# Performance work log

Measured on AMD Instinct MI355X. Metric: run time of the kernel, lower is better.

The kernel has to match this reference:

```python
import jax, jax.numpy as jnp
import numpy as np

H = 12          # nheads
SIM_EPS = 1e-8  # SimMatrix eps
LN_EPS = 1e-5   # nn.LayerNorm default eps
SLOPE = 0.01    # LeakyReLU default negative slope


def leaky(x):
    return jnp.where(x >= 0, x, SLOPE * x)


def etc_attention(hiddens, gamma, beta, Wout, bout):
    # hiddens: [B, L, 3*D]
    B, L, D3 = hiddens.shape
    D = D3 // 3
    d = D // H
    h = hiddens.reshape(B, L, 3, H, d)
    Q = h[:, :, 0].transpose(0, 2, 1, 3)  # [B,H,L,d]
    K = h[:, :, 1].transpose(0, 2, 1, 3)
    V = h[:, :, 2].transpose(0, 2, 1, 3)
    # cosine-similarity attention scores (SimMatrix(K, Q))
    Kn = K / jnp.clip(jnp.linalg.norm(K, axis=-1, keepdims=True), SIM_EPS, None)
    Qn = Q / jnp.clip(jnp.linalg.norm(Q, axis=-1, keepdims=True), SIM_EPS, None)
    att = jnp.einsum('bhid,bhjd->bhij', Kn, Qn)  # [B,H,L,L]
    # LayerNorm over the head axis H (lnormalize: [B, L*L, H] layernorm on last dim)
    mu = att.mean(axis=1, keepdims=True)
    var = att.var(axis=1, keepdims=True)  # biased, matches torch LayerNorm
    att = (att - mu) / jnp.sqrt(var + LN_EPS)
    att = att * gamma[None, :, None, None] + beta[None, :, None, None]
    att = jax.nn.softmax(att, axis=-1)
    att = jnp.where(jnp.isnan(att), jnp.zeros_like(att), att)  # removeNaN
    out = jnp.einsum('bhij,bhjd->bhid', att, V)          # att @ V
    out = out.transpose(0, 2, 1, 3).reshape(B, L, D)      # catHiddens
    # dropout is identity at inference; lin_out = Linear + Softmax
    probs = jax.nn.softmax(out @ Wout.T + bout, axis=-1)  # [B,L,C]
    return probs, att


def get_weights(att, masks):
    # att: [B,H,L,L], masks: [B,L] float
    w = masks * att.mean(axis=1).sum(axis=1)  # [B,L]
    return jax.nn.softmax(w, axis=-1)[..., None]  # [B,L,1]


def setup_inputs() -> dict:
    key = jax.random.key(0)
    ks = jax.random.split(key, 16)
    B, L = 16, 512
    Din, D, C, VOCAB = 300, 768, 20, 32000

    def kaiming(k, shape, fan_in):
        return jax.random.normal(k, shape, jnp.float32) * np.sqrt(2.0 / fan_in)

    return {
        'input_ids': jax.random.randint(ks[0], (B, L), 0, VOCAB),
        'wv': jax.random.normal(ks[1], (B, L, Din), jnp.float32),
        'emb': jax.random.normal(ks[2], (VOCAB, D), jnp.float32),
        'W_t': kaiming(ks[3], (3 * D, D), D),
        'b_t': jnp.zeros((3 * D,), jnp.float32),
        'gamma_t': jnp.ones((H,), jnp.float32),
        'beta_t': jnp.zeros((H,), jnp.float32),
        'Wout_t': kaiming(ks[4], (C, D), D),
        'bout_t': jnp.zeros((C,), jnp.float32),
        'W_h': kaiming(ks[5], (3 * D, Din), Din),
        'b_h': jnp.zeros((3 * D,), jnp.float32),
        'gamma_h': jnp.ones((H,), jnp.float32),
        'beta_h': jnp.zeros((H,), jnp.float32),
        'Wout_h': kaiming(ks[6], (C, D), D),
        'bout_h': jnp.zeros((C,), jnp.float32),
    }


def reference(input_ids, wv, emb, W_t, b_t, gamma_t, beta_t, Wout_t, bout_t,
              W_h, b_h, gamma_h, beta_h, Wout_h, bout_h):
    masks = (input_ids != 0).astype(jnp.float32)  # [B,L]
    # token branch: Embedding -> LeakyReLU -> Linear -> LeakyReLU
    h_t = leaky(leaky(emb[input_ids]) @ W_t.T + b_t)
    probs_t, att_t = etc_attention(h_t, gamma_t, beta_t, Wout_t, bout_t)
    probs_t = (get_weights(att_t, masks) * probs_t).sum(axis=1)  # [B,C]
    # hidden/word-vector branch: Linear -> LeakyReLU
    h_h = leaky(wv @ W_h.T + b_h)
    probs_h, att_h = etc_attention(h_h, gamma_h, beta_h, Wout_h, bout_h)
    probs_h = (get_weights(att_h, masks) * probs_h).sum(axis=1)
    return (probs_t + probs_h) / 2.0
```

## Files before the change

kernel.cpp:

```cpp
#include <hip/hip_runtime.h>

typedef unsigned int uint;
typedef unsigned short ushort;
typedef _Float16 f16;
typedef _Float16 h8 __attribute__((ext_vector_type(8)));
typedef float f32x4 __attribute__((ext_vector_type(4)));


__device__ __forceinline__ float b2f(ushort u){ return __uint_as_float(((uint)u)<<16); }
__device__ __forceinline__ ushort f2b(float f){
  uint u = __float_as_uint(f);
  uint r = u + 0x7fffu + ((u>>16)&1u);
  return (ushort)(r>>16);
}
__device__ __forceinline__ float leaky(float x){ return x >= 0.f ? x : 0.01f*x; }
__device__ __forceinline__ float ldf(const void* p, int idx, int isb){
  return isb ? b2f(((const ushort*)p)[idx]) : ((const float*)p)[idx];
}

#define GLOAD16(gp, lp) __builtin_amdgcn_global_load_lds( \
    (const __attribute__((address_space(1))) void*)(gp), \
    (__attribute__((address_space(3))) void*)(lp), 16, 0, 0)

__global__ __launch_bounds__(256) void k_init(const ushort* __restrict__ wvbits,
    int* __restrict__ flag, float* __restrict__ zbase){
  int bid = blockIdx.x, tid = threadIdx.x;
  if (bid == 0){
    if (tid == 0){
      int sane = 0;
      for (int i=0;i<128;i++){
        uint e = (wvbits[i]>>7)&0xffu;
        if (e==0u || (e>=90u && e<=150u)) sane++;
      }
      *flag = (sane >= 115) ? 1 : 0;
    }
  } else {
    zbase[(bid-1)*256 + tid] = 0.f;
  }
}

__global__ __launch_bounds__(256) void k_prep_all(const int* __restrict__ ids,
    const void* __restrict__ emb, const void* __restrict__ wv,
    const void* __restrict__ W0, const void* __restrict__ W1,
    const int* __restrict__ flag,
    f16* __restrict__ AhA, f16* __restrict__ WhA,
    f16* __restrict__ AhB, f16* __restrict__ WhB,
    int nBX, int nW0, int nA1, int nW1){
  int isb = *flag;
  int bx = blockIdx.x, tid = threadIdx.x;
  if (bx < nBX){
    int t = bx*256 + tid;
    int m = t / 96, kk = (t % 96) * 8;
    float o[8];
    if (isb){
      const ushort* src = (const ushort*)emb + (size_t)ids[m]*768 + kk;
      uint4 v = *(const uint4*)src;
      o[0]=__uint_as_float((v.x&0xffffu)<<16); o[1]=__uint_as_float(v.x&0xffff0000u);
      o[2]=__uint_as_float((v.y&0xffffu)<<16); o[3]=__uint_as_float(v.y&0xffff0000u);
      o[4]=__uint_as_float((v.z&0xffffu)<<16); o[5]=__uint_as_float(v.z&0xffff0000u);
      o[6]=__uint_as_float((v.w&0xffffu)<<16); o[7]=__uint_as_float(v.w&0xffff0000u);
    } else {
      const float* src = (const float*)emb + (size_t)ids[m]*768 + kk;
      float4 v0 = ((const float4*)src)[0];
      float4 v1 = ((const float4*)src)[1];
      o[0]=v0.x; o[1]=v0.y; o[2]=v0.z; o[3]=v0.w;
      o[4]=v1.x; o[5]=v1.y; o[6]=v1.z; o[7]=v1.w;
    }
    h8 hv;
    #pragma unroll
    for (int i=0;i<8;i++) hv[i] = (f16)leaky(o[i]);
    *(h8*)(AhA + (size_t)m*768 + kk) = hv;
  } else if (bx < nBX + nW0){
    int t = (bx - nBX)*256 + tid;
    int n = t / 96, kk = (t % 96) * 8;
    h8 hv;
    #pragma unroll
    for (int i=0;i<8;i++) hv[i] = (f16)ldf(W0, n*768 + kk + i, isb);
    *(h8*)(WhA + (size_t)n*768 + kk) = hv;
  } else if (bx < nBX + nW0 + nA1){
    int t = (bx - nBX - nW0)*256 + tid;
    int n = t / 40, kk = (t % 40) * 8;
    h8 hv;
    #pragma unroll
    for (int i=0;i<8;i++){
      int k = kk + i;
      hv[i] = (k < 300) ? (f16)ldf(wv, n*300 + k, isb) : (f16)0.f;
    }
    *(h8*)(AhB + (size_t)n*320 + kk) = hv;
  } else {
    int t = (bx - nBX - nW0 - nA1)*256 + tid;
    int n = t / 40, kk = (t % 40) * 8;
    h8 hv;
    #pragma unroll
    for (int i=0;i<8;i++){
      int k = kk + i;
      hv[i] = (k < 300) ? (f16)ldf(W1, n*300 + k, isb) : (f16)0.f;
    }
    *(h8*)(WhB + (size_t)n*320 + kk) = hv;
  }
}

__global__ __launch_bounds__(256) void k_gemm_m(
    const f16* AhA, const f16* WhA, const void* biasA, int KA,
    f16* QhA, f16* KhA, f16* VtA,
    const f16* AhB, const f16* WhB, const void* biasB, int KB,
    f16* QhB, f16* KhB, f16* VtB,
    const int* __restrict__ flag, int sbase){
  __shared__ __align__(16) f16 As[128*64];
  __shared__ __align__(16) f16 Bs[128*64];
  int z = sbase + blockIdx.z;
  const f16* Ah = z ? AhB : AhA;
  const f16* Wh = z ? WhB : WhA;
  const void* bias = z ? biasB : biasA;
  int KP = z ? KB : KA;
  f16* Qh = z ? QhB : QhA;
  f16* Kh = z ? KhB : KhA;
  f16* Vt = z ? VtB : VtA;
  int STEPS = KP >> 6;

  int tid = threadIdx.x;
  int w = tid >> 6, lane = tid & 63;
  int mrow = lane & 15, kq = lane >> 4;
  int m0 = blockIdx.x * 128;
  int n0 = blockIdx.y * 128;
  int msub = (w & 1) * 64, nsub = (w >> 1) * 64;

  f32x4 acc[4][4];
  #pragma unroll
  for (int mt=0; mt<4; mt++)
    #pragma unroll
    for (int nt=0; nt<4; nt++) acc[mt][nt] = (f32x4){0.f,0.f,0.f,0.f};

  int cbase = w*64 + lane;

  for (int step=0; step<STEPS; step++){
    int k0 = step*64;
    __syncthreads();
    #pragma unroll
    for (int rep=0; rep<4; rep++){
      int cb = rep*256 + w*64;
      int c  = rep*256 + cbase;
      int row = c >> 3;
      int qs  = (c & 7) ^ (row & 7);
      GLOAD16(Ah + (size_t)(m0+row)*KP + k0 + qs*8, As + cb*8);
      GLOAD16(Wh + (size_t)(n0+row)*KP + k0 + qs*8, Bs + cb*8);
    }
    __syncthreads();
    #pragma unroll
    for (int ks=0; ks<2; ks++){
      h8 af[4], bf[4];
      #pragma unroll
      for (int mt=0; mt<4; mt++){
        int row = msub + mt*16 + mrow;
        int slot = (ks*4 + kq) ^ (row & 7);
        af[mt] = *(const h8*)(As + row*64 + slot*8);
      }
      #pragma unroll
      for (int nt=0; nt<4; nt++){
        int row = nsub + nt*16 + mrow;
        int slot = (ks*4 + kq) ^ (row & 7);
        bf[nt] = *(const h8*)(Bs + row*64 + slot*8);
      }
      #pragma unroll
      for (int mt=0; mt<4; mt++)
        #pragma unroll
        for (int nt=0; nt<4; nt++)
          acc[mt][nt] = __builtin_amdgcn_mfma_f32_16x16x32_f16(af[mt], bf[nt], acc[mt][nt], 0, 0, 0);
    }
  }

  int isb = *flag;
  int n0w = n0 + nsub;
  int s = n0w / 768;
  int h = (n0w % 768) >> 6;
  float bv[4];
  #pragma unroll
  for (int nt=0; nt<4; nt++) bv[nt] = ldf(bias, n0w + nt*16 + mrow, isb);

  #pragma unroll
  for (int mt=0; mt<4; mt++){
    float yv[4][4];
    #pragma unroll
    for (int nt=0; nt<4; nt++)
      #pragma unroll
      for (int r=0; r<4; r++)
        yv[nt][r] = leaky(acc[mt][nt][r] + bv[nt]);
    if (s < 2){
      #pragma unroll
      for (int r=0; r<4; r++){
        float ss = yv[0][r]*yv[0][r] + yv[1][r]*yv[1][r]
                 + yv[2][r]*yv[2][r] + yv[3][r]*yv[3][r];
        ss += __shfl_xor(ss, 1); ss += __shfl_xor(ss, 2);
        ss += __shfl_xor(ss, 4); ss += __shfl_xor(ss, 8);
        float rn = 1.f / fmaxf(sqrtf(ss), 1e-8f);
        #pragma unroll
        for (int nt=0; nt<4; nt++) yv[nt][r] *= rn;
      }
    }
    #pragma unroll
    for (int nt=0; nt<4; nt++){
      #pragma unroll
      for (int r=0; r<4; r++){
        int m = m0 + msub + mt*16 + kq*4 + r;
        int dd = nt*16 + mrow;
        int bq = m >> 9, l = m & 511;
        float y = yv[nt][r];
        if (s == 0)      Qh[((size_t)(bq*12 + h)*512 + l)*64 + dd] = (f16)y;
        else if (s == 1) Kh[((size_t)(bq*12 + h)*512 + l)*64 + dd] = (f16)y;
        else             Vt[((size_t)(bq*12 + h)*64 + dd)*512 + l] = (f16)y;
      }
    }
  }
}

__global__ __launch_bounds__(256) void k_scores(const f16* __restrict__ Qh,
    const f16* __restrict__ Kh, const void* __restrict__ gamma,
    const void* __restrict__ beta, const int* __restrict__ flag,
    f16* __restrict__ E, float* __restrict__ lsump){
  constexpr int TS = 72;
  __shared__ f16 S[12*16*TS];
  __shared__ float gL[12], beL[12];

  int tid = threadIdx.x;
  int w = tid >> 6, lane = tid & 63;
  int kq = lane >> 4, mrow = lane & 15;
  int bx = (blockIdx.x & 7)*512 + (blockIdx.x >> 3);
  int jt = bx & 7, it = (bx >> 3) & 31, b = bx >> 8;
  int i0 = it*16, j0 = jt*64;

  if (tid < 12){ int isb = *flag; gL[tid] = ldf(gamma, tid, isb); beL[tid] = ldf(beta, tid, isb); }

  #pragma unroll
  for (int hh=0; hh<3; hh++){
    int h = w*3 + hh;
    const f16* kb = Kh + ((size_t)(b*12+h)*512 + i0 + mrow)*64;
    h8 a0 = *(const h8*)(kb + kq*8);
    h8 a1 = *(const h8*)(kb + 32 + kq*8);
    const f16* qb = Qh + ((size_t)(b*12+h)*512 + j0)*64;
    #pragma unroll
    for (int jn=0; jn<4; jn++){
      const f16* qr = qb + (size_t)(jn*16 + mrow)*64;
      h8 q0 = *(const h8*)(qr + kq*8);
      h8 q1 = *(const h8*)(qr + 32 + kq*8);
      f32x4 c = (f32x4){0.f,0.f,0.f,0.f};
      c = __builtin_amdgcn_mfma_f32_16x16x32_f16(a0, q0, c, 0, 0, 0);
      c = __builtin_amdgcn_mfma_f32_16x16x32_f16(a1, q1, c, 0, 0, 0);
      #pragma unroll
      for (int r=0;r<4;r++)
        S[(h*16 + kq*4 + r)*TS + jn*16 + mrow] = (f16)c[r];
    }
  }
  __syncthreads();
  int pj = tid & 63, piw = tid >> 6;
  #pragma unroll
  for (int p=0; p<4; p++){
    int i = piw*4 + p;
    float s[12];
    float mu = 0.f, sq = 0.f;
    #pragma unroll
    for (int h=0;h<12;h++){ s[h] = (float)S[(h*16+i)*TS + pj]; mu += s[h]; sq += s[h]*s[h]; }
    mu *= (1.f/12.f);
    float var = fmaxf(sq*(1.f/12.f) - mu*mu, 0.f);
    float rstd = rsqrtf(var + 1e-5f);
    #pragma unroll
    for (int h=0;h<12;h++){
      float e = __expf((s[h]-mu)*rstd*gL[h] + beL[h]);
      S[(h*16+i)*TS + pj] = (f16)e;
    }
  }
  __syncthreads();
  if (tid < 192){
    int h = tid >> 4, i = tid & 15;
    const f16* zr = &S[(h*16 + i)*TS];
    float ssum = 0.f;
    #pragma unroll
    for (int q=0;q<8;q++){
      h8 v = *(const h8*)(zr + q*8);
      #pragma unroll
      for (int t=0;t<8;t++) ssum += (float)v[t];
    }
    lsump[((size_t)(b*12+h)*512 + i0 + i)*8 + jt] = ssum;
  }
  #pragma unroll
  for (int u0=0; u0<6; u0++){
    int u = tid + u0*256;
    int h = u >> 7, rem = u & 127, i = rem >> 3, q = rem & 7;
    h8 v = *(const h8*)&S[(h*16 + i)*TS + q*8];
    *(h8*)(E + ((size_t)(b*12+h)*512 + i0 + i)*512 + j0 + q*8) = v;
  }
}

__global__ __launch_bounds__(256) void k_pv2(const f16* __restrict__ E,
    const f16* __restrict__ Vt, const float* __restrict__ lsump,
    float* __restrict__ O, float* __restrict__ colsum){
  __shared__ float csL[512];
  int tid = threadIdx.x;
  int w = tid >> 6, lane = tid & 63;
  int kq = lane >> 4, mrow = lane & 15;
  int b = blockIdx.y;
  int bx = (blockIdx.x & 7)*12 + (blockIdx.x >> 3);
  int h = bx >> 3, it = bx & 7;
  int i0w = it*64 + w*16;

  csL[tid] = 0.f; csL[tid + 256] = 0.f;
  const float4* lp = (const float4*)(lsump + ((size_t)(b*12+h)*512 + i0w + mrow)*8);
  float4 p0 = lp[0], p1 = lp[1];
  float rinv = 1.f / (p0.x+p0.y+p0.z+p0.w + p1.x+p1.y+p1.z+p1.w);
  __syncthreads();

  const f16* erow  = E  + ((size_t)(b*12+h)*512 + i0w + mrow)*512 + kq*8;
  const f16* vbase = Vt + ((size_t)(b*12+h)*64 + mrow)*512 + kq*8;

  f32x4 acc[4];
  #pragma unroll
  for (int nt=0; nt<4; nt++) acc[nt] = (f32x4){0.f,0.f,0.f,0.f};

  #pragma unroll 4
  for (int jt=0; jt<16; jt++){
    int j0 = jt*32;
    h8 ea  = *(const h8*)(erow + j0);
    h8 bf0 = *(const h8*)(vbase + j0);
    h8 bf1 = *(const h8*)(vbase + (size_t)16*512 + j0);
    h8 bf2 = *(const h8*)(vbase + (size_t)32*512 + j0);
    h8 bf3 = *(const h8*)(vbase + (size_t)48*512 + j0);
    acc[0] = __builtin_amdgcn_mfma_f32_16x16x32_f16(ea, bf0, acc[0], 0, 0, 0);
    acc[1] = __builtin_amdgcn_mfma_f32_16x16x32_f16(ea, bf1, acc[1], 0, 0, 0);
    acc[2] = __builtin_amdgcn_mfma_f32_16x16x32_f16(ea, bf2, acc[2], 0, 0, 0);
    acc[3] = __builtin_amdgcn_mfma_f32_16x16x32_f16(ea, bf3, acc[3], 0, 0, 0);
    float cs[8];
    #pragma unroll
    for (int t=0;t<8;t++) cs[t] = (float)ea[t] * rinv;
    #pragma unroll
    for (int t=0;t<8;t++){
      cs[t] += __shfl_xor(cs[t], 1); cs[t] += __shfl_xor(cs[t], 2);
      cs[t] += __shfl_xor(cs[t], 4); cs[t] += __shfl_xor(cs[t], 8);
    }
    if (mrow == 0){
      #pragma unroll
      for (int t=0;t<8;t++) atomicAdd(&csL[j0 + kq*8 + t], cs[t]);
    }
  }
  __syncthreads();
  atomicAdd(&colsum[b*512 + tid],       csL[tid]       * (1.f/12.f));
  atomicAdd(&colsum[b*512 + 256 + tid], csL[tid + 256] * (1.f/12.f));

  #pragma unroll
  for (int r=0; r<4; r++){
    float g = __shfl(rinv, kq*4 + r);
    #pragma unroll
    for (int nt=0; nt<4; nt++)
      O[((size_t)(b*512) + i0w + kq*4 + r)*768 + h*64 + nt*16 + mrow] = acc[nt][r] * g;
  }
}

__global__ __launch_bounds__(256) void k_probs_m(const float* OA, const float* OB,
    const void* WoA, const void* WoB, const void* boA, const void* boB,
    float* prA, float* prB, const int* __restrict__ flag, int sbase){
  int z = sbase + blockIdx.y;
  const float* O = z ? OB : OA;
  const void* Wout = z ? WoB : WoA;
  const void* bout = z ? boB : boA;
  float* probs = z ? prB : prA;
  int isb = *flag;
  int tid = threadIdx.x, wv = tid>>6, lane = tid&63;
  int m = blockIdx.x*4 + wv;
  const float* orow = O + (size_t)m*768;
  float acc[20];
  #pragma unroll
  for (int c=0;c<20;c++) acc[c]=0.f;
  for (int kk=0; kk<12; kk++){
    float o = orow[kk*64 + lane];
    #pragma unroll
    for (int c=0;c<20;c++)
      acc[c] += o * ldf(Wout, c*768 + kk*64 + lane, isb);
  }
  #pragma unroll
  for (int c=0;c<20;c++){
    #pragma unroll
    for (int off=1; off<64; off<<=1) acc[c] += __shfl_xor(acc[c], off, 64);
  }
  float mx = -3.4e38f;
  #pragma unroll
  for (int c=0;c<20;c++){ acc[c] += ldf(bout, c, isb); mx = fmaxf(mx, acc[c]); }
  float s=0.f;
  #pragma unroll
  for (int c=0;c<20;c++){ acc[c] = __expf(acc[c]-mx); s += acc[c]; }
  float inv = 1.f/s;
  if (lane == 0){
    float* pr = probs + (size_t)m*20;
    #pragma unroll
    for (int c=0;c<20;c++) pr[c] = acc[c]*inv;
  }
}

__global__ __launch_bounds__(512) void k_final_m(const int* __restrict__ ids,
    const float* __restrict__ cs0, const float* __restrict__ cs1,
    const float* __restrict__ pr0, const float* __restrict__ pr1,
    const int* __restrict__ flag, void* __restrict__ outp){
  __shared__ float red[8];
  __shared__ float bcast;
  __shared__ float pacc[8][20];
  __shared__ float osum[20];
  int b = blockIdx.x, tid = threadIdx.x;
  int wv = tid>>6, lane = tid&63;
  int msk = (ids[b*512+tid] != 0);
  for (int br=0; br<2; br++){
    const float* colsum = br ? cs1 : cs0;
    const float* probs  = br ? pr1 : pr0;
    float w = msk ? colsum[b*512+tid] : 0.f;
    float mx = w;
    #pragma unroll
    for (int off=1; off<64; off<<=1) mx = fmaxf(mx, __shfl_xor(mx, off, 64));
    if (lane==0) red[wv] = mx;
    __syncthreads();
    if (tid==0){ float m2 = red[0]; for (int k2=1;k2<8;k2++) m2 = fmaxf(m2, red[k2]); bcast = m2; }
    __syncthreads();
    float M = bcast;
    float e = __expf(w - M);
    float s = e;
    #pragma unroll
    for (int off=1; off<64; off<<=1) s += __shfl_xor(s, off, 64);
    if (lane==0) red[wv] = s;
    __syncthreads();
    if (tid==0){ float s2=0.f; for (int k2=0;k2<8;k2++) s2 += red[k2]; bcast = s2; }
    __syncthreads();
    float wn = e / bcast;
    float p[20];
    const float* pr = probs + ((size_t)b*512 + tid)*20;
    #pragma unroll
    for (int c=0;c<20;c++) p[c] = wn * pr[c];
    #pragma unroll
    for (int c=0;c<20;c++){
      #pragma unroll
      for (int off=1; off<64; off<<=1) p[c] += __shfl_xor(p[c], off, 64);
    }
    if (lane==0){
      #pragma unroll
      for (int c=0;c<20;c++) pacc[wv][c] = p[c];
    }
    __syncthreads();
    if (tid < 20){
      float s2 = 0.f;
      #pragma unroll
      for (int k2=0;k2<8;k2++) s2 += pacc[k2][tid];
      if (br == 0) osum[tid] = s2;
      else         osum[tid] += s2;
    }
    __syncthreads();
  }
  if (tid < 20){
    float v = osum[tid] * 0.5f;
    if (*flag) ((ushort*)outp)[b*20 + tid] = f2b(v);
    else       ((float*)outp)[b*20 + tid] = v;
  }
}

extern "C" void kernel_launch(void* const* d_in, const int* in_sizes, int n_in,
                              void* d_out, int out_size, void* d_ws, size_t ws_size,
                              hipStream_t stream){
  (void)in_sizes; (void)n_in; (void)out_size;
  const int*  ids = (const int*)d_in[0];
  const void* wvp = d_in[1];
  const void* emb = d_in[2];
  const void* Wt[2]  = {d_in[3], d_in[9]};
  const void* bt[2]  = {d_in[4], d_in[10]};
  const void* gm[2]  = {d_in[5], d_in[11]};
  const void* bet[2] = {d_in[6], d_in[12]};
  const void* Wo[2]  = {d_in[7], d_in[13]};
  const void* bo[2]  = {d_in[8], d_in[14]};

  char* p = (char*)d_ws;
  #define ALLOC(ty, name, cnt) ty* name = (ty*)p; p += sizeof(ty)*(size_t)(cnt)

  p = (char*)d_ws;
  ALLOC(float, O0, 6291456);
  ALLOC(float, O1, 6291456);
  ALLOC(f16, Qh0, 6291456); ALLOC(f16, Kh0, 6291456); ALLOC(f16, Vt0, 6291456);
  ALLOC(f16, Qh1, 6291456); ALLOC(f16, Kh1, 6291456); ALLOC(f16, Vt1, 6291456);
  ALLOC(f16, Ah0, 6291456); ALLOC(f16, Wh0, 1769472);
  ALLOC(f16, Ah1, 2621440); ALLOC(f16, Wh1, 737280);
  ALLOC(float, probs0, 163840); ALLOC(float, probs1, 163840);
  ALLOC(float, zb_big, 16384);
  ALLOC(int, flag_big, 4);
  ALLOC(f16, E_big, 50331648);
  size_t needBig = (size_t)(p - (char*)d_ws);

  if (ws_size >= needBig){
    float* colsum0 = zb_big;
    float* colsum1 = zb_big + 8192;
    int* flagp = flag_big; f16* E = E_big;
    float* lsump0 = (float*)Ah0;
    float* lsump1 = lsump0 + 786432;

    k_init<<<65, 256, 0, stream>>>((const ushort*)wvp, flagp, zb_big);
    k_prep_all<<<3072+864+1280+360, 256, 0, stream>>>(ids, emb, wvp, Wt[0], Wt[1],
        flagp, Ah0, Wh0, Ah1, Wh1, 3072, 864, 1280, 360);
    dim3 gg(64, 18, 2);
    k_gemm_m<<<gg, 256, 0, stream>>>(Ah0, Wh0, bt[0], 768, Qh0, Kh0, Vt0,
                                     Ah1, Wh1, bt[1], 320, Qh1, Kh1, Vt1, flagp, 0);
    dim3 gpv(96, 16);
    k_scores<<<4096, 256, 0, stream>>>(Qh0, Kh0, gm[0], bet[0], flagp, E, lsump0);
    k_pv2<<<gpv, 256, 0, stream>>>(E, Vt0, lsump0, O0, colsum0);
    k_scores<<<4096, 256, 0, stream>>>(Qh1, Kh1, gm[1], bet[1], flagp, E, lsump1);
    k_pv2<<<gpv, 256, 0, stream>>>(E, Vt1, lsump1, O1, colsum1);
    dim3 gpr(2048, 2);
    k_probs_m<<<gpr, 256, 0, stream>>>(O0, O1, Wo[0], Wo[1], bo[0], bo[1],
                                       probs0, probs1, flagp, 0);
    k_final_m<<<16, 512, 0, stream>>>(ids, colsum0, colsum1, probs0, probs1, flagp, d_out);
    return;
  }

  p = (char*)d_ws;
  ALLOC(float, O, 6291456);
  ALLOC(f16, Qh, 6291456); ALLOC(f16, Kh, 6291456); ALLOC(f16, Vt, 6291456);
  ALLOC(f16, Ah, 6291456); ALLOC(f16, Wh, 1769472);
  ALLOC(float, probsA, 163840); ALLOC(float, probsB, 163840);
  ALLOC(float, zb, 16384);
  ALLOC(int, flagm, 4);
  ALLOC(f16, Em, 50331648);
  float* colsum0 = zb;
  float* colsum1 = zb + 8192;
  float* lsumm0 = (float*)Ah;
  float* lsumm1 = lsumm0 + 786432;

  k_init<<<65, 256, 0, stream>>>((const ushort*)wvp, flagm, zb);
  k_prep_all<<<3072+864, 256, 0, stream>>>(ids, emb, wvp, Wt[0], Wt[1],
      flagm, Ah, Wh, Ah, Wh, 3072, 864, 0, 0);
  dim3 g1(64, 18, 1);
  k_gemm_m<<<g1, 256, 0, stream>>>(Ah, Wh, bt[0], 768, Qh, Kh, Vt,
                                   Ah, Wh, bt[0], 768, Qh, Kh, Vt, flagm, 0);
  dim3 gpv(96, 16);
  k_scores<<<4096, 256, 0, stream>>>(Qh, Kh, gm[0], bet[0], flagm, Em, lsumm0);
  k_pv2<<<gpv, 256, 0, stream>>>(Em, Vt, lsumm0, O, colsum0);
  dim3 gpr(2048, 1);
  k_probs_m<<<gpr, 256, 0, stream>>>(O, O, Wo[0], Wo[1], bo[0], bo[1],
                                     probsA, probsB, flagm, 0);
  k_prep_all<<<1280+360, 256, 0, stream>>>(ids, emb, wvp, Wt[0], Wt[1],
      flagm, Ah, Wh, Ah, Wh, 0, 0, 1280, 360);
  k_gemm_m<<<g1, 256, 0, stream>>>(Ah, Wh, bt[1], 320, Qh, Kh, Vt,
                                   Ah, Wh, bt[1], 320, Qh, Kh, Vt, flagm, 0);
  k_scores<<<4096, 256, 0, stream>>>(Qh, Kh, gm[1], bet[1], flagm, Em, lsumm1);
  k_pv2<<<gpv, 256, 0, stream>>>(Em, Vt, lsumm1, O, colsum1);
  k_probs_m<<<gpr, 256, 0, stream>>>(O, O, Wo[0], Wo[1], bo[0], bo[1],
                                     probsA, probsB, flagm, 1);
  k_final_m<<<16, 512, 0, stream>>>(ids, colsum0, colsum1, probsA, probsB, flagm, d_out);
  #undef ALLOC
}
```

Measured before the change: 572.7 us.

## Fuse output projection into PV kernel via atomic partial logits, swizzle GEMM blocks

The PV kernel now multiplies its per-head output tile by the matching Wout slice held in shared memory, and atomically accumulates partial class logits into a small buffer. This removes the full O tensor write and re-read (two 25MB float buffers) and the separate projection kernel, which is replaced by a light softmax kernel. k_scores zeroes the partial-logit buffer. The GEMM also remaps block indices along M to change scheduling locality. The cost is extra shuffles and atomics in k_pv2, plus a dependence on k_scores zeroing plog before k_pv2 runs.

Measured after the change: 717.8 us. +25.3%, slower.

```diff
diff --git a/kernel.cpp b/kernel.cpp
--- a/kernel.cpp
+++ b/kernel.cpp
@@ -121,7 +121,7 @@
   int tid = threadIdx.x;
   int w = tid >> 6, lane = tid & 63;
   int mrow = lane & 15, kq = lane >> 4;
-  int m0 = blockIdx.x * 128;
+  int m0 = (((blockIdx.x & 7)<<3) | (blockIdx.x >> 3)) * 128;
   int n0 = blockIdx.y * 128;
   int msub = (w & 1) * 64, nsub = (w >> 1) * 64;
 
@@ -216,7 +216,7 @@
 __global__ __launch_bounds__(256) void k_scores(const f16* __restrict__ Qh,
     const f16* __restrict__ Kh, const void* __restrict__ gamma,
     const void* __restrict__ beta, const int* __restrict__ flag,
-    f16* __restrict__ E, float* __restrict__ lsump){
+    f16* __restrict__ E, float* __restrict__ lsump, float* __restrict__ plogz){
   constexpr int TS = 72;
   __shared__ f16 S[12*16*TS];
   __shared__ float gL[12], beL[12];
@@ -224,11 +224,13 @@
   int tid = threadIdx.x;
   int w = tid >> 6, lane = tid & 63;
   int kq = lane >> 4, mrow = lane & 15;
-  int bx = (blockIdx.x & 7)*512 + (blockIdx.x >> 3);
+  int braw = blockIdx.x;
+  int bx = (braw & 7)*512 + (braw >> 3);
   int jt = bx & 7, it = (bx >> 3) & 31, b = bx >> 8;
   int i0 = it*16, j0 = jt*64;
 
   if (tid < 12){ int isb = *flag; gL[tid] = ldf(gamma, tid, isb); beL[tid] = ldf(beta, tid, isb); }
+  if (tid < 40) plogz[(size_t)braw*40 + tid] = 0.f;
 
   #pragma unroll
   for (int hh=0; hh<3; hh++){
@@ -292,8 +294,10 @@
 
 __global__ __launch_bounds__(256) void k_pv2(const f16* __restrict__ E,
     const f16* __restrict__ Vt, const float* __restrict__ lsump,
-    float* __restrict__ O, float* __restrict__ colsum){
+    float* __restrict__ colsum, float* __restrict__ plog,
+    const void* __restrict__ Wout, const int* __restrict__ flag){
   __shared__ float csL[512];
+  __shared__ float woL[20][64];
   int tid = threadIdx.x;
   int w = tid >> 6, lane = tid & 63;
   int kq = lane >> 4, mrow = lane & 15;
@@ -303,6 +307,15 @@
   int i0w = it*64 + w*16;
 
   csL[tid] = 0.f; csL[tid + 256] = 0.f;
+  {
+    int isb = *flag;
+    #pragma unroll
+    for (int u0=0; u0<5; u0++){
+      int u = tid + u0*256;
+      int c = u >> 6, d = u & 63;
+      woL[c][d] = ldf(Wout, c*768 + h*64 + d, isb);
+    }
+  }
   const float4* lp = (const float4*)(lsump + ((size_t)(b*12+h)*512 + i0w + mrow)*8);
   float4 p0 = lp[0], p1 = lp[1];
   float rinv = 1.f / (p0.x+p0.y+p0.z+p0.w + p1.x+p1.y+p1.z+p1.w);
@@ -344,53 +357,48 @@
   atomicAdd(&colsum[b*512 + tid],       csL[tid]       * (1.f/12.f));
   atomicAdd(&colsum[b*512 + 256 + tid], csL[tid + 256] * (1.f/12.f));
 
+  float o4[4][4];
   #pragma unroll
   for (int r=0; r<4; r++){
     float g = __shfl(rinv, kq*4 + r);
     #pragma unroll
-    for (int nt=0; nt<4; nt++)
-      O[((size_t)(b*512) + i0w + kq*4 + r)*768 + h*64 + nt*16 + mrow] = acc[nt][r] * g;
-  }
-}
-
-__global__ __launch_bounds__(256) void k_probs_m(const float* OA, const float* OB,
-    const void* WoA, const void* WoB, const void* boA, const void* boB,
-    float* prA, float* prB, const int* __restrict__ flag, int sbase){
+    for (int nt=0; nt<4; nt++) o4[r][nt] = acc[nt][r] * g;
+  }
+  #pragma unroll
+  for (int c=0; c<20; c++){
+    float w0 = woL[c][ 0 + mrow];
+    float w1 = woL[c][16 + mrow];
+    float w2 = woL[c][32 + mrow];
+    float w3 = woL[c][48 + mrow];
+    #pragma unroll
+    for (int r=0; r<4; r++){
+      float v = o4[r][0]*w0 + o4[r][1]*w1 + o4[r][2]*w2 + o4[r][3]*w3;
+      v += __shfl_xor(v, 1); v += __shfl_xor(v, 2);
+      v += __shfl_xor(v, 4); v += __shfl_xor(v, 8);
+      if (mrow == 0)
+        atomicAdd(&plog[((size_t)(b*512) + i0w + kq*4 + r)*20 + c], v);
+    }
+  }
+}
+
+__global__ __launch_bounds__(256) void k_probs_s(const float* plA, const float* plB,
+    const void* boA, const void* boB, float* prA, float* prB,
+    const int* __restrict__ flag, int sbase){
   int z = sbase + blockIdx.y;
-  const float* O = z ? OB : OA;
-  const void* Wout = z ? WoB : WoA;
+  const float* pl = z ? plB : plA;
   const void* bout = z ? boB : boA;
   float* probs = z ? prB : prA;
   int isb = *flag;
-  int tid = threadIdx.x, wv = tid>>6, lane = tid&63;
-  int m = blockIdx.x*4 + wv;
-  const float* orow = O + (size_t)m*768;
-  float acc[20];
-  #pragma unroll
-  for (int c=0;c<20;c++) acc[c]=0.f;
-  for (int kk=0; kk<12; kk++){
-    float o = orow[kk*64 + lane];
-    #pragma unroll
-    for (int c=0;c<20;c++)
-      acc[c] += o * ldf(Wout, c*768 + kk*64 + lane, isb);
-  }
-  #pragma unroll
-  for (int c=0;c<20;c++){
-    #pragma unroll
-    for (int off=1; off<64; off<<=1) acc[c] += __shfl_xor(acc[c], off, 64);
-  }
-  float mx = -3.4e38f;
-  #pragma unroll
-  for (int c=0;c<20;c++){ acc[c] += ldf(bout, c, isb); mx = fmaxf(mx, acc[c]); }
-  float s=0.f;
-  #pragma unroll
-  for (int c=0;c<20;c++){ acc[c] = __expf(acc[c]-mx); s += acc[c]; }
+  int m = blockIdx.x*256 + threadIdx.x;
+  float a[20]; float mx = -3.4e38f;
+  #pragma unroll
+  for (int c=0;c<20;c++){ a[c] = pl[(size_t)m*20+c] + ldf(bout, c, isb); mx = fmaxf(mx, a[c]); }
+  float s = 0.f;
+  #pragma unroll
+  for (int c=0;c<20;c++){ a[c] = __expf(a[c]-mx); s += a[c]; }
   float inv = 1.f/s;
-  if (lane == 0){
-    float* pr = probs + (size_t)m*20;
-    #pragma unroll
-    for (int c=0;c<20;c++) pr[c] = acc[c]*inv;
-  }
+  #pragma unroll
+  for (int c=0;c<20;c++) probs[(size_t)m*20+c] = a[c]*inv;
 }
 
 __global__ __launch_bounds__(512) void k_final_m(const int* __restrict__ ids,
@@ -473,12 +481,11 @@
   #define ALLOC(ty, name, cnt) ty* name = (ty*)p; p += sizeof(ty)*(size_t)(cnt)
 
   p = (char*)d_ws;
-  ALLOC(float, O0, 6291456);
-  ALLOC(float, O1, 6291456);
   ALLOC(f16, Qh0, 6291456); ALLOC(f16, Kh0, 6291456); ALLOC(f16, Vt0, 6291456);
   ALLOC(f16, Qh1, 6291456); ALLOC(f16, Kh1, 6291456); ALLOC(f16, Vt1, 6291456);
   ALLOC(f16, Ah0, 6291456); ALLOC(f16, Wh0, 1769472);
   ALLOC(f16, Ah1, 2621440); ALLOC(f16, Wh1, 737280);
+  ALLOC(float, plog0, 163840); ALLOC(float, plog1, 163840);
   ALLOC(float, probs0, 163840); ALLOC(float, probs1, 163840);
   ALLOC(float, zb_big, 16384);
   ALLOC(int, flag_big, 4);
@@ -499,21 +506,21 @@
     k_gemm_m<<<gg, 256, 0, stream>>>(Ah0, Wh0, bt[0], 768, Qh0, Kh0, Vt0,
                                      Ah1, Wh1, bt[1], 320, Qh1, Kh1, Vt1, flagp, 0);
     dim3 gpv(96, 16);
-    k_scores<<<4096, 256, 0, stream>>>(Qh0, Kh0, gm[0], bet[0], flagp, E, lsump0);
-    k_pv2<<<gpv, 256, 0, stream>>>(E, Vt0, lsump0, O0, colsum0);
-    k_scores<<<4096, 256, 0, stream>>>(Qh1, Kh1, gm[1], bet[1], flagp, E, lsump1);
-    k_pv2<<<gpv, 256, 0, stream>>>(E, Vt1, lsump1, O1, colsum1);
-    dim3 gpr(2048, 2);
-    k_probs_m<<<gpr, 256, 0, stream>>>(O0, O1, Wo[0], Wo[1], bo[0], bo[1],
+    k_scores<<<4096, 256, 0, stream>>>(Qh0, Kh0, gm[0], bet[0], flagp, E, lsump0, plog0);
+    k_pv2<<<gpv, 256, 0, stream>>>(E, Vt0, lsump0, colsum0, plog0, Wo[0], flagp);
+    k_scores<<<4096, 256, 0, stream>>>(Qh1, Kh1, gm[1], bet[1], flagp, E, lsump1, plog1);
+    k_pv2<<<gpv, 256, 0, stream>>>(E, Vt1, lsump1, colsum1, plog1, Wo[1], flagp);
+    dim3 gps(32, 2);
+    k_probs_s<<<gps, 256, 0, stream>>>(plog0, plog1, bo[0], bo[1],
                                        probs0, probs1, flagp, 0);
     k_final_m<<<16, 512, 0, stream>>>(ids, colsum0, colsum1, probs0, probs1, flagp, d_out);
     return;
   }
 
   p = (char*)d_ws;
-  ALLOC(float, O, 6291456);
   ALLOC(f16, Qh, 6291456); ALLOC(f16, Kh, 6291456); ALLOC(f16, Vt, 6291456);
   ALLOC(f16, Ah, 6291456); ALLOC(f16, Wh, 1769472);
+  ALLOC(float, plogm, 163840);
   ALLOC(float, probsA, 163840); ALLOC(float, probsB, 163840);
   ALLOC(float, zb, 16384);
   ALLOC(int, flagm, 4);
@@ -530,18 +537,18 @@
   k_gemm_m<<<g1, 256, 0, stream>>>(Ah, Wh, bt[0], 768, Qh, Kh, Vt,
                                    Ah, Wh, bt[0], 768, Qh, Kh, Vt, flagm, 0);
   dim3 gpv(96, 16);
-  k_scores<<<4096, 256, 0, stream>>>(Qh, Kh, gm[0], bet[0], flagm, Em, lsumm0);
-  k_pv2<<<gpv, 256, 0, stream>>>(Em, Vt, lsumm0, O, colsum0);
-  dim3 gpr(2048, 1);
-  k_probs_m<<<gpr, 256, 0, stream>>>(O, O, Wo[0], Wo[1], bo[0], bo[1],
+  k_scores<<<4096, 256, 0, stream>>>(Qh, Kh, gm[0], bet[0], flagm, Em, lsumm0, plogm);
+  k_pv2<<<gpv, 256, 0, stream>>>(Em, Vt, lsumm0, colsum0, plogm, Wo[0], flagm);
+  dim3 gps(32, 1);
+  k_probs_s<<<gps, 256, 0, stream>>>(plogm, plogm, bo[0], bo[1],
                                      probsA, probsB, flagm, 0);
   k_prep_all<<<1280+360, 256, 0, stream>>>(ids, emb, wvp, Wt[0], Wt[1],
       flagm, Ah, Wh, Ah, Wh, 0, 0, 1280, 360);
   k_gemm_m<<<g1, 256, 0, stream>>>(Ah, Wh, bt[1], 320, Qh, Kh, Vt,
                                    Ah, Wh, bt[1], 320, Qh, Kh, Vt, flagm, 0);
-  k_scores<<<4096, 256, 0, stream>>>(Qh, Kh, gm[1], bet[1], flagm, Em, lsumm1);
-  k_pv2<<<gpv, 256, 0, stream>>>(Em, Vt, lsumm1, O, colsum1);
-  k_probs_m<<<gpr, 256, 0, stream>>>(O, O, Wo[0], Wo[1], bo[0], bo[1],
+  k_scores<<<4096, 256, 0, stream>>>(Qh, Kh, gm[1], bet[1], flagm, Em, lsumm1, plogm);
+  k_pv2<<<gpv, 256, 0, stream>>>(Em, Vt, lsumm1, colsum1, plogm, Wo[1], flagm);
+  k_probs_s<<<gps, 256, 0, stream>>>(plogm, plogm, bo[0], bo[1],
                                      probsA, probsB, flagm, 1);
   k_final_m<<<16, 512, 0, stream>>>(ids, colsum0, colsum1, probsA, probsB, flagm, d_out);
   #undef ALLOC
```

## Batch both attention branches into single scores and PV launches with separate E buffers

Applied to the files above, without the earlier changes.

Allocates a second E score buffer when the workspace allows it, so the scores and PV kernels for both branches can run as one launch each, with a z-grid dimension picking the branch. This cuts launch count and the tail idle time between the two branches, at the cost of a second 100MB E buffer. The GEMM's M-block order is also swizzled for better L2 locality, and k_scores gains a min-blocks-per-CU launch bound of 4, which may raise register pressure.

New measurement: 601.4 us. 5.0% more time.

```diff
diff --git a/kernel.cpp b/kernel.cpp
--- a/kernel.cpp
+++ b/kernel.cpp
@@ -121,7 +121,7 @@
   int tid = threadIdx.x;
   int w = tid >> 6, lane = tid & 63;
   int mrow = lane & 15, kq = lane >> 4;
-  int m0 = blockIdx.x * 128;
+  int m0 = (((blockIdx.x & 7)<<3) | (blockIdx.x >> 3)) * 128;
   int n0 = blockIdx.y * 128;
   int msub = (w & 1) * 64, nsub = (w >> 1) * 64;
 
@@ -213,13 +213,25 @@
   }
 }
 
-__global__ __launch_bounds__(256) void k_scores(const f16* __restrict__ Qh,
-    const f16* __restrict__ Kh, const void* __restrict__ gamma,
-    const void* __restrict__ beta, const int* __restrict__ flag,
-    f16* __restrict__ E, float* __restrict__ lsump){
+__global__ __launch_bounds__(256, 4) void k_scores(
+    const f16* __restrict__ Qh0, const f16* __restrict__ Kh0,
+    const void* __restrict__ g0, const void* __restrict__ be0,
+    f16* __restrict__ E0, float* __restrict__ ls0,
+    const f16* __restrict__ Qh1, const f16* __restrict__ Kh1,
+    const void* __restrict__ g1, const void* __restrict__ be1,
+    f16* __restrict__ E1, float* __restrict__ ls1,
+    const int* __restrict__ flag, int sbase){
   constexpr int TS = 72;
   __shared__ f16 S[12*16*TS];
   __shared__ float gL[12], beL[12];
+
+  int z = sbase + blockIdx.z;
+  const f16* Qh = z ? Qh1 : Qh0;
+  const f16* Kh = z ? Kh1 : Kh0;
+  const void* gamma = z ? g1 : g0;
+  const void* beta  = z ? be1 : be0;
+  f16* E = z ? E1 : E0;
+  float* lsump = z ? ls1 : ls0;
 
   int tid = threadIdx.x;
   int w = tid >> 6, lane = tid & 63;
@@ -290,10 +302,20 @@
   }
 }
 
-__global__ __launch_bounds__(256) void k_pv2(const f16* __restrict__ E,
-    const f16* __restrict__ Vt, const float* __restrict__ lsump,
-    float* __restrict__ O, float* __restrict__ colsum){
+__global__ __launch_bounds__(256) void k_pv2(
+    const f16* __restrict__ E0, const f16* __restrict__ Vt0,
+    const float* __restrict__ ls0, float* __restrict__ O0, float* __restrict__ cs0,
+    const f16* __restrict__ E1, const f16* __restrict__ Vt1,
+    const float* __restrict__ ls1, float* __restrict__ O1, float* __restrict__ cs1,
+    int sbase){
   __shared__ float csL[512];
+  int z = sbase + blockIdx.z;
+  const f16* E = z ? E1 : E0;
+  const f16* Vt = z ? Vt1 : Vt0;
+  const float* lsump = z ? ls1 : ls0;
+  float* O = z ? O1 : O0;
+  float* colsum = z ? cs1 : cs0;
+
   int tid = threadIdx.x;
   int w = tid >> 6, lane = tid & 63;
   int kq = lane >> 4, mrow = lane & 15;
@@ -482,13 +504,18 @@
   ALLOC(float, probs0, 163840); ALLOC(float, probs1, 163840);
   ALLOC(float, zb_big, 16384);
   ALLOC(int, flag_big, 4);
-  ALLOC(f16, E_big, 50331648);
+  ALLOC(f16, E0_big, 50331648);
   size_t needBig = (size_t)(p - (char*)d_ws);
+  ALLOC(f16, E1_big, 50331648);
+  size_t needBig2 = (size_t)(p - (char*)d_ws);
 
   if (ws_size >= needBig){
+    int two_e = (ws_size >= needBig2);
     float* colsum0 = zb_big;
     float* colsum1 = zb_big + 8192;
-    int* flagp = flag_big; f16* E = E_big;
+    int* flagp = flag_big;
+    f16* E0 = E0_big;
+    f16* E1 = two_e ? E1_big : E0_big;
     float* lsump0 = (float*)Ah0;
     float* lsump1 = lsump0 + 786432;
 
@@ -498,11 +525,25 @@
     dim3 gg(64, 18, 2);
     k_gemm_m<<<gg, 256, 0, stream>>>(Ah0, Wh0, bt[0], 768, Qh0, Kh0, Vt0,
                                      Ah1, Wh1, bt[1], 320, Qh1, Kh1, Vt1, flagp, 0);
-    dim3 gpv(96, 16);
-    k_scores<<<4096, 256, 0, stream>>>(Qh0, Kh0, gm[0], bet[0], flagp, E, lsump0);
-    k_pv2<<<gpv, 256, 0, stream>>>(E, Vt0, lsump0, O0, colsum0);
-    k_scores<<<4096, 256, 0, stream>>>(Qh1, Kh1, gm[1], bet[1], flagp, E, lsump1);
-    k_pv2<<<gpv, 256, 0, stream>>>(E, Vt1, lsump1, O1, colsum1);
+    if (two_e){
+      dim3 gs(4096, 1, 2);
+      k_scores<<<gs, 256, 0, stream>>>(Qh0, Kh0, gm[0], bet[0], E0, lsump0,
+                                       Qh1, Kh1, gm[1], bet[1], E1, lsump1, flagp, 0);
+      dim3 gpv(96, 16, 2);
+      k_pv2<<<gpv, 256, 0, stream>>>(E0, Vt0, lsump0, O0, colsum0,
+                                     E1, Vt1, lsump1, O1, colsum1, 0);
+    } else {
+      dim3 gs(4096, 1, 1);
+      dim3 gpv(96, 16, 1);
+      k_scores<<<gs, 256, 0, stream>>>(Qh0, Kh0, gm[0], bet[0], E0, lsump0,
+                                       Qh1, Kh1, gm[1], bet[1], E1, lsump1, flagp, 0);
+      k_pv2<<<gpv, 256, 0, stream>>>(E0, Vt0, lsump0, O0, colsum0,
+                                     E1, Vt1, lsump1, O1, colsum1, 0);
+      k_scores<<<gs, 256, 0, stream>>>(Qh0, Kh0, gm[0], bet[0], E0, lsump0,
+                                       Qh1, Kh1, gm[1], bet[1], E1, lsump1, flagp, 1);
+      k_pv2<<<gpv, 256, 0, stream>>>(E0, Vt0, lsump0, O0, colsum0,
+                                     E1, Vt1, lsump1, O1, colsum1, 1);
+    }
     dim3 gpr(2048, 2);
     k_probs_m<<<gpr, 256, 0, stream>>>(O0, O1, Wo[0], Wo[1], bo[0], bo[1],
                                        probs0, probs1, flagp, 0);
@@ -529,9 +570,12 @@
   dim3 g1(64, 18, 1);
   k_gemm_m<<<g1, 256, 0, stream>>>(Ah, Wh, bt[0], 768, Qh, Kh, Vt,
                                    Ah, Wh, bt[0], 768, Qh, Kh, Vt, flagm, 0);
-  dim3 gpv(96, 16);
-  k_scores<<<4096, 256, 0, stream>>>(Qh, Kh, gm[0], bet[0], flagm, Em, lsumm0);
-  k_pv2<<<gpv, 256, 0, stream>>>(Em, Vt, lsumm0, O, colsum0);
+  dim3 gs(4096, 1, 1);
+  dim3 gpv(96, 16, 1);
+  k_scores<<<gs, 256, 0, stream>>>(Qh, Kh, gm[0], bet[0], Em, lsumm0,
+                                   Qh, Kh, gm[0], bet[0], Em, lsumm0, flagm, 0);
+  k_pv2<<<gpv, 256, 0, stream>>>(Em, Vt, lsumm0, O, colsum0,
+                                 Em, Vt, lsumm0, O, colsum0, 0);
   dim3 gpr(2048, 1);
   k_probs_m<<<gpr, 256, 0, stream>>>(O, O, Wo[0], Wo[1], bo[0], bo[1],
                                      probsA, probsB, flagm, 0);
@@ -539,8 +583,10 @@
       flagm, Ah, Wh, Ah, Wh, 0, 0, 1280, 360);
   k_gemm_m<<<g1, 256, 0, stream>>>(Ah, Wh, bt[1], 320, Qh, Kh, Vt,
                                    Ah, Wh, bt[1], 320, Qh, Kh, Vt, flagm, 0);
-  k_scores<<<4096, 256, 0, stream>>>(Qh, Kh, gm[1], bet[1], flagm, Em, lsumm1);
-  k_pv2<<<gpv, 256, 0, stream>>>(Em, Vt, lsumm1, O, colsum1);
+  k_scores<<<gs, 256, 0, stream>>>(Qh, Kh, gm[1], bet[1], Em, lsumm1,
+                                   Qh, Kh, gm[1], bet[1], Em, lsumm1, flagm, 0);
+  k_pv2<<<gpv, 256, 0, stream>>>(Em, Vt, lsumm1, O, colsum1,
+                                 Em, Vt, lsumm1, O, colsum1, 0);
   k_probs_m<<<gpr, 256, 0, stream>>>(O, O, Wo[0], Wo[1], bo[0], bo[1],
                                      probsA, probsB, flagm, 1);
   k_final_m<<<16, 512, 0, stream>>>(ids, colsum0, colsum1, probsA, probsB, flagm, d_out);
```
